# Optimization experiments

Measured on AMD Instinct MI355X. Metric: run time of the kernel, lower is better.

The kernel has to match this reference:

```python
import jax, jax.numpy as jnp
import numpy as np

ALPHA = 0.5   # leak rate
GAMMA = 0.01  # input scaling
RHO = 1.0     # target spectral radius
SPARSITY = 0.9  # fraction of zeros in W

T, N_INPUT, N_OUTPUT = 4096, 8192, 2048


def setup_inputs() -> dict:
    key = jax.random.key(0)
    k1, k2, k3, k4 = jax.random.split(key, 4)
    x = jax.random.normal(k1, (T, N_INPUT), dtype=jnp.float32)
    Win = GAMMA * jax.random.normal(k2, (N_INPUT, N_OUTPUT), dtype=jnp.float32)
    mask = (jax.random.uniform(k3, (N_OUTPUT, N_OUTPUT)) < (1.0 - SPARSITY)).astype(jnp.float32)
    W0 = jax.random.normal(k4, (N_OUTPUT, N_OUTPUT), dtype=jnp.float32) * mask
    # spectral-radius normalization (circular-law estimate: radius ~ sqrt(p * N) for
    # density p), standing in for rho * W / max|eig(W)| at init time.
    W = RHO * W0 / jnp.sqrt((1.0 - SPARSITY) * N_OUTPUT)
    return {"x": x, "W": W, "Win": Win}


def reference(x, W, Win):
    # x: [T, nInput]; output: [T, nOutput] (stacked hidden states)
    u_proj = x @ Win  # [T, nOutput], input projection is independent of the recurrence

    def step(v, up):
        # v: [nOutput]  leaky-integrator reservoir update
        v_new = (1.0 - ALPHA) * v + ALPHA * jnp.tanh(v @ W + up)
        return v_new, v_new

    v0 = jnp.zeros((W.shape[0],), dtype=x.dtype)  # ESN starts from zero state
    _, vs = jax.lax.scan(step, v0, u_proj)
    return vs
```

## Files before the change

kernel.cpp:

```cpp
#include <hip/hip_runtime.h>
#include <hip/hip_bf16.h>
#include <math.h>

#define T_STEPS 4096
#define N_IN    8192
#define N_OUT   2048

#define RB    64
#define CPB   32
#define GRP   8
#define CAP   288
#define KMAX  (CAP / GRP)
#define NMT   32
#define GEMM_BLOCKS 128
#define GM_BK 32

#define SM_ENT   0
#define SM_CNTS  73728
#define SM_VSH   (73728 + 128)
#define SM_BYTES (73728 + 128 + 16384)
#define SM_GA    0
#define SM_GB    16896

__device__ __forceinline__ float fast_tanh(float x) {
    const float ax = fabsf(x);
    const float e  = __expf(2.0f * ax);
    const float r  = __builtin_amdgcn_rcpf(e + 1.0f);
    const float t  = 1.0f - 2.0f * r;
    return copysignf(t, x);
}

__global__ __launch_bounds__(256, 1) void esn_fused(
        const float* __restrict__ X,
        const float* __restrict__ W,
        const float* __restrict__ Win,
        float* __restrict__ UO,
        unsigned long long* vslots,
        int* mcnt) {
    __shared__ __align__(16) char smem[SM_BYTES];
    const int tid = threadIdx.x;

    if (blockIdx.x >= RB) {
        float (*As)[132] = reinterpret_cast<float(*)[132]>(smem + SM_GA);
        float (*Bs)[132] = reinterpret_cast<float(*)[132]>(smem + SM_GB);
        const int gb = (int)blockIdx.x - RB;
        const int K = N_IN, N = N_OUT;
        const int tx = tid & 15;
        const int ty = tid >> 4;

#pragma unroll 1
        for (int s = 0; s < 4; ++s) {
            const int tile = gb + 128 * s;
            const int bm = tile >> 4;
            const int bn = tile & 15;

            float acc[8][8];
#pragma unroll
            for (int i = 0; i < 8; i++)
#pragma unroll
                for (int jj = 0; jj < 8; jj++) acc[i][jj] = 0.f;

            const float* Xb = X + (size_t)(bm * 128) * K;
            const float* Wb = Win + bn * 128;

            for (int kt = 0; kt < K; kt += GM_BK) {
#pragma unroll
                for (int q = 0; q < 4; q++) {
                    const int r  = (tid >> 3) + q * 32;
                    const int c4 = (tid & 7) * 4;
                    const float4 a4 = *reinterpret_cast<const float4*>(&Xb[(size_t)r * K + kt + c4]);
                    As[c4 + 0][r] = a4.x;
                    As[c4 + 1][r] = a4.y;
                    As[c4 + 2][r] = a4.z;
                    As[c4 + 3][r] = a4.w;
                }
#pragma unroll
                for (int q = 0; q < 4; q++) {
                    const int r  = (tid >> 5) + q * 8;
                    const int c4 = (tid & 31) * 4;
                    *reinterpret_cast<float4*>(&Bs[r][c4]) =
                        *reinterpret_cast<const float4*>(&Wb[(size_t)(kt + r) * N + c4]);
                }
                __syncthreads();

#pragma unroll
                for (int k = 0; k < GM_BK; k++) {
                    float a[8], bb[8];
#pragma unroll
                    for (int i = 0; i < 4; i++) {
                        a[i]     = As[k][ty * 4 + i];
                        a[4 + i] = As[k][64 + ty * 4 + i];
                    }
#pragma unroll
                    for (int jj = 0; jj < 4; jj++) {
                        bb[jj]     = Bs[k][tx * 4 + jj];
                        bb[4 + jj] = Bs[k][64 + tx * 4 + jj];
                    }
#pragma unroll
                    for (int i = 0; i < 8; i++)
#pragma unroll
                        for (int jj = 0; jj < 8; jj++)
                            acc[i][jj] = fmaf(a[i], bb[jj], acc[i][jj]);
                }
                __syncthreads();
            }

#pragma unroll
            for (int i = 0; i < 8; i++) {
                const int mr = bm * 128 + ((i < 4) ? (ty * 4 + i) : (64 + ty * 4 + (i - 4)));
                float* Crow = UO + (size_t)mr * N + bn * 128;
                float4 v0 = make_float4(acc[i][0], acc[i][1], acc[i][2], acc[i][3]);
                float4 v1 = make_float4(acc[i][4], acc[i][5], acc[i][6], acc[i][7]);
                *reinterpret_cast<float4*>(&Crow[tx * 4])      = v0;
                *reinterpret_cast<float4*>(&Crow[64 + tx * 4]) = v1;
            }
            __syncthreads();
            if (tid == 0)
                __hip_atomic_fetch_add(&mcnt[bm], 1, __ATOMIC_RELEASE,
                                       __HIP_MEMORY_SCOPE_AGENT);
            __syncthreads();
        }
        return;
    }

    __builtin_amdgcn_s_setprio(1);
    auto ent  = reinterpret_cast<unsigned long long(*)[CAP]>(smem + SM_ENT);
    int* cnts = reinterpret_cast<int*>(smem + SM_CNTS);
    float (*vsh)[N_OUT] = reinterpret_cast<float(*)[N_OUT]>(smem + SM_VSH);

    const int b   = blockIdx.x;
    const int c   = tid >> 3;
    const int l   = tid & 7;
    const int j   = b * CPB + c;
    const int lw  = tid & 63;

    int cnt = 0;
    for (int k = 0; k < N_OUT / GRP; k++) {
        const float w = W[(size_t)(l + GRP * k) * N_OUT + j];
        cnt += (w != 0.0f) ? 1 : 0;
    }
    int inc = cnt;
#pragma unroll
    for (int d = 1; d < GRP; d <<= 1) {
        int n = __shfl_up(inc, d, 64);
        if (l >= d) inc += n;
    }
    int pos = inc - cnt;
    if (l == GRP - 1) cnts[c] = inc;
    for (int k = 0; k < N_OUT / GRP; k++) {
        const int i = l + GRP * k;
        const float w = W[(size_t)i * N_OUT + j];
        if (w != 0.0f) {
            if (pos < CAP)
                ent[c][pos] = ((unsigned long long)(unsigned)i << 32) | __float_as_uint(w);
            pos++;
        }
    }
    __syncthreads();
    const int ccnt = min(cnts[c], CAP);

    float wreg[KMAX];
    int   ireg[KMAX];
#pragma unroll
    for (int k = 0; k < KMAX; k++) {
        const int p = l + k * GRP;
        if (p < ccnt) {
            const unsigned long long e = ent[c][p];
            wreg[k] = __uint_as_float((unsigned)e);
            ireg[k] = (int)(e >> 32);
        } else {
            wreg[k] = 0.f;
            ireg[k] = 0;
        }
    }

    int kmw = (ccnt + GRP - 1) >> 3;
#pragma unroll
    for (int d = 1; d < 64; d <<= 1) {
        const int o = __shfl_xor(kmw, d, 64);
        kmw = (o > kmw) ? o : kmw;
    }
    if (kmw > KMAX) kmw = KMAX;

#pragma unroll
    for (int pass = 0; pass < KMAX; ++pass) {
#pragma unroll
        for (int i = (pass & 1); i + 1 < KMAX; i += 2) {
            const int ka = (wreg[i]     == 0.f) ? 64 : (((ireg[i]     & 31) - lw) & 31);
            const int kb = (wreg[i + 1] == 0.f) ? 64 : (((ireg[i + 1] & 31) - lw) & 31);
            const bool sw = ka > kb;
            const int   ti = sw ? ireg[i] : ireg[i + 1];
            const int   bi = sw ? ireg[i + 1] : ireg[i];
            const float tw = sw ? wreg[i] : wreg[i + 1];
            const float bw = sw ? wreg[i + 1] : wreg[i];
            ireg[i] = bi; ireg[i + 1] = ti;
            wreg[i] = bw; wreg[i + 1] = tw;
        }
    }

    float vold = 0.f;

#pragma unroll 1
    for (int t = 0; t < T_STEPS; t++) {
        if ((t & 127) == 0) {
            while (__hip_atomic_load(&mcnt[t >> 7], __ATOMIC_ACQUIRE,
                                     __HIP_MEMORY_SCOPE_AGENT) < 16) { }
        }
        float u = 0.f;
        if (l == 0) u = UO[(size_t)t * N_OUT + j];

        unsigned long long* vin = vslots + (size_t)(t & 1) * N_OUT;
        float* dst = vsh[t & 1];
        unsigned long long uq[8];
#pragma unroll
        for (int q = 0; q < 8; q++)
            uq[q] = __hip_atomic_load(&vin[tid + q * 256], __ATOMIC_RELAXED,
                                      __HIP_MEMORY_SCOPE_AGENT);
        unsigned pend = 0xFFu;
#pragma unroll 1
        while (true) {
            unsigned np = 0;
#pragma unroll
            for (int q = 0; q < 8; q++) {
                if (pend & (1u << q)) {
                    if ((unsigned)(uq[q] >> 32) == (unsigned)t)
                        dst[tid + q * 256] = __uint_as_float((unsigned)uq[q]);
                    else
                        np |= (1u << q);
                }
            }
            pend = np;
            if (!pend) break;
#pragma unroll
            for (int q = 0; q < 8; q++)
                if (pend & (1u << q))
                    uq[q] = __hip_atomic_load(&vin[tid + q * 256], __ATOMIC_RELAXED,
                                              __HIP_MEMORY_SCOPE_AGENT);
        }
        __syncthreads();

        const float* vcur = vsh[t & 1];
        float yy[4] = {0.f, 0.f, 0.f, 0.f};
#define MACK(k) yy[(k) & 3] = fmaf(wreg[(k)], vcur[ireg[(k)]], yy[(k) & 3])
#pragma unroll
        for (int k = 0; k < 20; k += 4) {
            MACK(k + 0); MACK(k + 1); MACK(k + 2); MACK(k + 3);
        }
        if (kmw > 20) { MACK(20); MACK(21); MACK(22); MACK(23); }
        if (kmw > 24) { MACK(24); MACK(25); MACK(26); MACK(27); }
        if (kmw > 28) { MACK(28); MACK(29); MACK(30); MACK(31); }
        if (kmw > 32) { MACK(32); MACK(33); MACK(34); MACK(35); }
#undef MACK
        float y = (yy[0] + yy[1]) + (yy[2] + yy[3]);
#pragma unroll
        for (int d = GRP / 2; d >= 1; d >>= 1) y += __shfl_xor(y, d, 64);

        if (l == 0) {
            const float vnew = 0.5f * vold + 0.5f * fast_tanh(y + u);
            vold = vnew;
            const unsigned long long slot =
                ((unsigned long long)(unsigned)(t + 1) << 32) | __float_as_uint(vnew);
            __hip_atomic_store(&vslots[(size_t)((t + 1) & 1) * N_OUT + j], slot,
                               __ATOMIC_RELAXED, __HIP_MEMORY_SCOPE_AGENT);
            UO[(size_t)t * N_OUT + j] = vnew;
        }
    }
}

extern "C" void kernel_launch(void* const* d_in, const int* in_sizes, int n_in,
                              void* d_out, int out_size, void* d_ws, size_t ws_size,
                              hipStream_t stream) {
    const float* x   = (const float*)d_in[0];
    const float* W   = (const float*)d_in[1];
    const float* Win = (const float*)d_in[2];
    float* out = (float*)d_out;

    unsigned long long* vslots = (unsigned long long*)d_ws;
    int* mcnt = (int*)((char*)d_ws + 2 * N_OUT * sizeof(unsigned long long));

    hipMemsetAsync(d_ws, 0,
                   2 * N_OUT * sizeof(unsigned long long) + NMT * sizeof(int),
                   stream);

    esn_fused<<<RB + GEMM_BLOCKS, 256, 0, stream>>>(x, W, Win, out, vslots, mcnt);
}
```

Baseline: 11.72 ms.

## Give each wavefront its own state copy to drop block barrier; one GEMM tile per block

Each wavefront now loads the full previous state vector from the global slots into its own private shared-memory copy. Because no other wavefront reads that copy, the per-step __syncthreads and the double-buffered shared state are removed, reusing the entry-list region once it has been consumed. In exchange, every wave issues four times as many global atomic loads per step and holds 32 in-flight 64-bit values in registers. Separately, the input-projection GEMM is spread over 512 blocks with one tile each instead of 128 blocks looping over four tiles.

After: 34.36 ms. +193.2%, slower.

```diff
diff --git a/kernel.cpp b/kernel.cpp
--- a/kernel.cpp
+++ b/kernel.cpp
@@ -12,13 +12,11 @@
 #define CAP   288
 #define KMAX  (CAP / GRP)
 #define NMT   32
-#define GEMM_BLOCKS 128
+#define GEMM_BLOCKS 512
 #define GM_BK 32
 
-#define SM_ENT   0
 #define SM_CNTS  73728
-#define SM_VSH   (73728 + 128)
-#define SM_BYTES (73728 + 128 + 16384)
+#define SM_BYTES (73728 + 128)
 #define SM_GA    0
 #define SM_GB    16896
 
@@ -44,95 +42,89 @@
         float (*As)[132] = reinterpret_cast<float(*)[132]>(smem + SM_GA);
         float (*Bs)[132] = reinterpret_cast<float(*)[132]>(smem + SM_GB);
         const int gb = (int)blockIdx.x - RB;
+        const int bm = gb >> 4;
+        const int bn = gb & 15;
         const int K = N_IN, N = N_OUT;
         const int tx = tid & 15;
         const int ty = tid >> 4;
 
-#pragma unroll 1
-        for (int s = 0; s < 4; ++s) {
-            const int tile = gb + 128 * s;
-            const int bm = tile >> 4;
-            const int bn = tile & 15;
-
-            float acc[8][8];
-#pragma unroll
-            for (int i = 0; i < 8; i++)
-#pragma unroll
-                for (int jj = 0; jj < 8; jj++) acc[i][jj] = 0.f;
-
-            const float* Xb = X + (size_t)(bm * 128) * K;
-            const float* Wb = Win + bn * 128;
-
-            for (int kt = 0; kt < K; kt += GM_BK) {
-#pragma unroll
-                for (int q = 0; q < 4; q++) {
-                    const int r  = (tid >> 3) + q * 32;
-                    const int c4 = (tid & 7) * 4;
-                    const float4 a4 = *reinterpret_cast<const float4*>(&Xb[(size_t)r * K + kt + c4]);
-                    As[c4 + 0][r] = a4.x;
-                    As[c4 + 1][r] = a4.y;
-                    As[c4 + 2][r] = a4.z;
-                    As[c4 + 3][r] = a4.w;
+        float acc[8][8];
+#pragma unroll
+        for (int i = 0; i < 8; i++)
+#pragma unroll
+            for (int jj = 0; jj < 8; jj++) acc[i][jj] = 0.f;
+
+        const float* Xb = X + (size_t)(bm * 128) * K;
+        const float* Wb = Win + bn * 128;
+
+        for (int kt = 0; kt < K; kt += GM_BK) {
+#pragma unroll
+            for (int q = 0; q < 4; q++) {
+                const int r  = (tid >> 3) + q * 32;
+                const int c4 = (tid & 7) * 4;
+                const float4 a4 = *reinterpret_cast<const float4*>(&Xb[(size_t)r * K + kt + c4]);
+                As[c4 + 0][r] = a4.x;
+                As[c4 + 1][r] = a4.y;
+                As[c4 + 2][r] = a4.z;
+                As[c4 + 3][r] = a4.w;
+            }
+#pragma unroll
+            for (int q = 0; q < 4; q++) {
+                const int r  = (tid >> 5) + q * 8;
+                const int c4 = (tid & 31) * 4;
+                *reinterpret_cast<float4*>(&Bs[r][c4]) =
+                    *reinterpret_cast<const float4*>(&Wb[(size_t)(kt + r) * N + c4]);
+            }
+            __syncthreads();
+
+#pragma unroll
+            for (int k = 0; k < GM_BK; k++) {
+                float a[8], bb[8];
+#pragma unroll
+                for (int i = 0; i < 4; i++) {
+                    a[i]     = As[k][ty * 4 + i];
+                    a[4 + i] = As[k][64 + ty * 4 + i];
                 }
 #pragma unroll
-                for (int q = 0; q < 4; q++) {
-                    const int r  = (tid >> 5) + q * 8;
-                    const int c4 = (tid & 31) * 4;
-                    *reinterpret_cast<float4*>(&Bs[r][c4]) =
-                        *reinterpret_cast<const float4*>(&Wb[(size_t)(kt + r) * N + c4]);
+                for (int jj = 0; jj < 4; jj++) {
+                    bb[jj]     = Bs[k][tx * 4 + jj];
+                    bb[4 + jj] = Bs[k][64 + tx * 4 + jj];
                 }
-                __syncthreads();
-
-#pragma unroll
-                for (int k = 0; k < GM_BK; k++) {
-                    float a[8], bb[8];
-#pragma unroll
-                    for (int i = 0; i < 4; i++) {
-                        a[i]     = As[k][ty * 4 + i];
-                        a[4 + i] = As[k][64 + ty * 4 + i];
-                    }
-#pragma unroll
-                    for (int jj = 0; jj < 4; jj++) {
-                        bb[jj]     = Bs[k][tx * 4 + jj];
-                        bb[4 + jj] = Bs[k][64 + tx * 4 + jj];
-                    }
-#pragma unroll
-                    for (int i = 0; i < 8; i++)
-#pragma unroll
-                        for (int jj = 0; jj < 8; jj++)
-                            acc[i][jj] = fmaf(a[i], bb[jj], acc[i][jj]);
-                }
-                __syncthreads();
-            }
-
-#pragma unroll
-            for (int i = 0; i < 8; i++) {
-                const int mr = bm * 128 + ((i < 4) ? (ty * 4 + i) : (64 + ty * 4 + (i - 4)));
-                float* Crow = UO + (size_t)mr * N + bn * 128;
-                float4 v0 = make_float4(acc[i][0], acc[i][1], acc[i][2], acc[i][3]);
-                float4 v1 = make_float4(acc[i][4], acc[i][5], acc[i][6], acc[i][7]);
-                *reinterpret_cast<float4*>(&Crow[tx * 4])      = v0;
-                *reinterpret_cast<float4*>(&Crow[64 + tx * 4]) = v1;
+#pragma unroll
+                for (int i = 0; i < 8; i++)
+#pragma unroll
+                    for (int jj = 0; jj < 8; jj++)
+                        acc[i][jj] = fmaf(a[i], bb[jj], acc[i][jj]);
             }
             __syncthreads();
-            if (tid == 0)
-                __hip_atomic_fetch_add(&mcnt[bm], 1, __ATOMIC_RELEASE,
-                                       __HIP_MEMORY_SCOPE_AGENT);
-            __syncthreads();
-        }
+        }
+
+#pragma unroll
+        for (int i = 0; i < 8; i++) {
+            const int mr = bm * 128 + ((i < 4) ? (ty * 4 + i) : (64 + ty * 4 + (i - 4)));
+            float* Crow = UO + (size_t)mr * N + bn * 128;
+            float4 v0 = make_float4(acc[i][0], acc[i][1], acc[i][2], acc[i][3]);
+            float4 v1 = make_float4(acc[i][4], acc[i][5], acc[i][6], acc[i][7]);
+            *reinterpret_cast<float4*>(&Crow[tx * 4])      = v0;
+            *reinterpret_cast<float4*>(&Crow[64 + tx * 4]) = v1;
+        }
+        __syncthreads();
+        if (tid == 0)
+            __hip_atomic_fetch_add(&mcnt[bm], 1, __ATOMIC_RELEASE,
+                                   __HIP_MEMORY_SCOPE_AGENT);
         return;
     }
 
     __builtin_amdgcn_s_setprio(1);
-    auto ent  = reinterpret_cast<unsigned long long(*)[CAP]>(smem + SM_ENT);
+    auto ent  = reinterpret_cast<unsigned long long(*)[CAP]>(smem);
     int* cnts = reinterpret_cast<int*>(smem + SM_CNTS);
-    float (*vsh)[N_OUT] = reinterpret_cast<float(*)[N_OUT]>(smem + SM_VSH);
 
     const int b   = blockIdx.x;
+    const int wv  = tid >> 6;
+    const int lw  = tid & 63;
     const int c   = tid >> 3;
     const int l   = tid & 7;
     const int j   = b * CPB + c;
-    const int lw  = tid & 63;
 
     int cnt = 0;
     for (int k = 0; k < N_OUT / GRP; k++) {
@@ -198,6 +190,8 @@
         }
     }
 
+    __syncthreads();
+    float* vshw = reinterpret_cast<float*>(smem) + wv * N_OUT;
     float vold = 0.f;
 
 #pragma unroll 1
@@ -209,22 +203,22 @@
         float u = 0.f;
         if (l == 0) u = UO[(size_t)t * N_OUT + j];
 
-        unsigned long long* vin = vslots + (size_t)(t & 1) * N_OUT;
-        float* dst = vsh[t & 1];
-        unsigned long long uq[8];
-#pragma unroll
-        for (int q = 0; q < 8; q++)
-            uq[q] = __hip_atomic_load(&vin[tid + q * 256], __ATOMIC_RELAXED,
+        const unsigned long long* vin = vslots + (size_t)(t & 1) * N_OUT;
+        const unsigned ut = (unsigned)t;
+        unsigned long long uq[32];
+#pragma unroll
+        for (int q = 0; q < 32; q++)
+            uq[q] = __hip_atomic_load(&vin[lw + q * 64], __ATOMIC_RELAXED,
                                       __HIP_MEMORY_SCOPE_AGENT);
-        unsigned pend = 0xFFu;
+        unsigned pend = 0xFFFFFFFFu;
 #pragma unroll 1
         while (true) {
             unsigned np = 0;
 #pragma unroll
-            for (int q = 0; q < 8; q++) {
+            for (int q = 0; q < 32; q++) {
                 if (pend & (1u << q)) {
-                    if ((unsigned)(uq[q] >> 32) == (unsigned)t)
-                        dst[tid + q * 256] = __uint_as_float((unsigned)uq[q]);
+                    if ((unsigned)(uq[q] >> 32) == ut)
+                        vshw[lw + q * 64] = __uint_as_float((unsigned)uq[q]);
                     else
                         np |= (1u << q);
                 }
@@ -232,16 +226,14 @@
             pend = np;
             if (!pend) break;
 #pragma unroll
-            for (int q = 0; q < 8; q++)
+            for (int q = 0; q < 32; q++)
                 if (pend & (1u << q))
-                    uq[q] = __hip_atomic_load(&vin[tid + q * 256], __ATOMIC_RELAXED,
+                    uq[q] = __hip_atomic_load(&vin[lw + q * 64], __ATOMIC_RELAXED,
                                               __HIP_MEMORY_SCOPE_AGENT);
         }
-        __syncthreads();
-
-        const float* vcur = vsh[t & 1];
+
         float yy[4] = {0.f, 0.f, 0.f, 0.f};
-#define MACK(k) yy[(k) & 3] = fmaf(wreg[(k)], vcur[ireg[(k)]], yy[(k) & 3])
+#define MACK(k) yy[(k) & 3] = fmaf(wreg[(k)], vshw[ireg[(k)]], yy[(k) & 3])
 #pragma unroll
         for (int k = 0; k < 20; k += 4) {
             MACK(k + 0); MACK(k + 1); MACK(k + 2); MACK(k + 3);
```
